# Performance work log

Hardware: AMD Instinct MI355X
Metric: run time of the kernel (lower is better)

The kernel has to match this reference:

```python
import jax, jax.numpy as jnp
import numpy as np
from jax import lax

IN_DIM = 256
MID = IN_DIM // 2          # 128
NUM_FILTERS = 8
OUT_DIM = 256
EMBED_DIM = 256
BN_EPS = 1e-5


def star_relu(x, scale, bias):
    # StarReLU: s * relu(x)**2 + b
    return scale * jnp.square(jax.nn.relu(x)) + bias


def setup_inputs() -> dict:
    key = jax.random.key(0)
    ks = jax.random.split(key, 12)
    B, H, W = 2, 16, 16
    h, w = 128, 128
    inp = {
        "x": jax.random.normal(ks[0], (B, IN_DIM, H, W), jnp.float32),
        "y": jax.random.normal(ks[1], (B, OUT_DIM, h, w), jnp.float32),
        # feature_fuse: 1x1 conv, depthwise 3x3 conv, BatchNorm (eval-mode stats)
        "conv1_w": jax.random.normal(ks[2], (MID, IN_DIM), jnp.float32) * 0.02,
        "conv1_b": jnp.zeros((MID,), jnp.float32),
        "dw_w": jax.random.normal(ks[3], (MID, 3, 3), jnp.float32) * 0.02,
        "dw_b": jnp.zeros((MID,), jnp.float32),
        "bn_gamma": jnp.ones((MID,), jnp.float32),
        "bn_beta": jnp.zeros((MID,), jnp.float32),
        "bn_mean": jax.random.normal(ks[4], (MID,), jnp.float32) * 0.1,
        "bn_var": jax.random.uniform(ks[5], (MID,), jnp.float32, 0.5, 1.5),
        "sr1_scale": jnp.ones((1,), jnp.float32),
        "sr1_bias": jnp.zeros((1,), jnp.float32),
        # channle_expand 1x1 conv
        "ce_w": jax.random.normal(ks[6], (NUM_FILTERS, MID), jnp.float32) * 0.02,
        "ce_b": jnp.zeros((NUM_FILTERS,), jnp.float32),
        "sr2_scale": jnp.ones((1,), jnp.float32),
        "sr2_bias": jnp.zeros((1,), jnp.float32),
        "W_base": jax.random.normal(ks[7], (OUT_DIM * EMBED_DIM, NUM_FILTERS), jnp.float32) * 0.02,
    }
    return inp


def reference(x, y, conv1_w, conv1_b, dw_w, dw_b, bn_gamma, bn_beta, bn_mean,
              bn_var, sr1_scale, sr1_bias, ce_w, ce_b, sr2_scale, sr2_bias, W_base):
    B, _, fh, fw = x.shape
    b, c, h, w = y.shape
    ph, pw = h // fh, w // fw

    # feature_fuse
    t = jnp.einsum('bchw,oc->bohw', x, conv1_w) + conv1_b[None, :, None, None]
    t = lax.conv_general_dilated(
        t, dw_w[:, None, :, :], (1, 1), ((1, 1), (1, 1)),
        feature_group_count=MID,
        dimension_numbers=('NCHW', 'OIHW', 'NCHW')) + dw_b[None, :, None, None]
    t = bn_gamma[None, :, None, None] * (t - bn_mean[None, :, None, None]) \
        * lax.rsqrt(bn_var + BN_EPS)[None, :, None, None] + bn_beta[None, :, None, None]
    t = star_relu(t, sr1_scale, sr1_bias)

    # channle_expand + act -> per-location filter coefficients [b, F, fh, fw]
    wdec = star_relu(jnp.einsum('bchw,fc->bfhw', t, ce_w) + ce_b[None, :, None, None],
                     sr2_scale, sr2_bias)

    # hypernetwork: [b, E*O, fh, fw], flattened as (embed_dim, out_dim)
    Wd = jnp.einsum('bfhw,ef->behw', wdec, W_base)
    Wd = Wd.reshape(b, EMBED_DIM, OUT_DIM, fh, fw)

    # massive-group 1x1 conv == per-(batch, block) small GEMM over spatial patches
    yb = y.reshape(b, c, fh, ph, fw, pw)
    out = jnp.einsum('beoij,boipjq->beipjq', Wd, yb)  # [b, E, fh, ph, fw, pw]
    return out.reshape(b, EMBED_DIM, h, w)
```

## Files before the change

### kernel.cpp

```cpp
#include <hip/hip_runtime.h>
#include <stdint.h>

typedef unsigned short u16t;
typedef unsigned int   u32t;
typedef __attribute__((ext_vector_type(8))) short short8;
typedef __attribute__((ext_vector_type(4))) float f32x4;

__device__ __forceinline__ float bf2f(u16t h){
  union { u32t u; float f; } c; c.u = ((u32t)h) << 16; return c.f;
}
__device__ __forceinline__ u16t f2bf(float f){
  union { float f; u32t u; } c; c.f = f;
  u32t u = c.u;
  u = u + 0x7fffu + ((u >> 16) & 1u);
  return (u16t)(u >> 16);
}
__device__ __forceinline__ u32t pk2(float a, float b){
  return (u32t)f2bf(a) | ((u32t)f2bf(b) << 16);
}

template<bool BF>
__device__ __forceinline__ float ldv(const void* p, size_t i){
  if constexpr (BF) return bf2f(((const u16t*)p)[i]);
  else              return ((const float*)p)[i];
}
template<bool BF>
__device__ __forceinline__ void ld8(const void* p, size_t i, float* v){
  if constexpr (BF){
    uint4 u = *(const uint4*)((const u16t*)p + i);
    const u32t a[4] = {u.x, u.y, u.z, u.w};
#pragma unroll
    for (int d = 0; d < 4; ++d){
      v[2*d]   = bf2f((u16t)(a[d] & 0xffffu));
      v[2*d+1] = bf2f((u16t)(a[d] >> 16));
    }
  } else {
    const float4* q = (const float4*)((const float*)p + i);
    float4 A = q[0], B = q[1];
    v[0]=A.x; v[1]=A.y; v[2]=A.z; v[3]=A.w;
    v[4]=B.x; v[5]=B.y; v[6]=B.z; v[7]=B.w;
  }
}
template<bool BF>
__device__ __forceinline__ void ld8pk(const void* p, size_t i, u32t* dst){
  if constexpr (BF){
    uint4 u = *(const uint4*)((const u16t*)p + i);
    dst[0]=u.x; dst[1]=u.y; dst[2]=u.z; dst[3]=u.w;
  } else {
    const float4* q = (const float4*)((const float*)p + i);
    float4 A = q[0], B = q[1];
    dst[0] = pk2(A.x, A.y); dst[1] = pk2(A.z, A.w);
    dst[2] = pk2(B.x, B.y); dst[3] = pk2(B.z, B.w);
  }
}

__global__ void k_probe(const void* xv, int* flag){
  __shared__ int cnt;
  const int t = threadIdx.x;
  if (t == 0) cnt = 0;
  __syncthreads();
  u16t h = ((const u16t*)xv)[t];
  int e = (h >> 7) & 0xff;
  if (e >= 90 && e <= 150) atomicAdd(&cnt, 1);
  __syncthreads();
  if (t == 0) *flag = (cnt >= 104) ? 1 : 0;
}

template<bool BF>
__device__ __forceinline__ void conv1_body(
    const void* x, const void* w, const void* bias, float* t1)
{
  __shared__ float xs[256];
  const int bid = blockIdx.x;
  const int b = bid >> 8, i = (bid >> 4) & 15, j = bid & 15;
  const int t = threadIdx.x;
  const size_t base = (size_t)b * 65536 + i * 16 + j;
  xs[t]       = ldv<BF>(x, base + (size_t)t * 256);
  xs[t + 128] = ldv<BF>(x, base + (size_t)(t + 128) * 256);
  __syncthreads();
  float acc = ldv<BF>(bias, t);
  for (int k = 0; k < 256; k += 8){
    float wv[8];
    ld8<BF>(w, (size_t)t * 256 + k, wv);
#pragma unroll
    for (int d = 0; d < 8; ++d) acc += xs[k + d] * wv[d];
  }
  t1[((size_t)(b * 128 + t) * 16 + i) * 16 + j] = acc;
}
__global__ __launch_bounds__(128) void k_conv1(
    const void* x, const void* w, const void* bias, float* t1, const int* flag){
  if (*flag) conv1_body<true >(x, w, bias, t1);
  else       conv1_body<false>(x, w, bias, t1);
}

template<bool BF>
__device__ __forceinline__ void wdec_body(
    const float* t1, const void* dww, const void* dwb,
    const void* bng, const void* bnb, const void* bnm, const void* bnv,
    const void* s1s, const void* s1b, const void* cew, const void* ceb,
    const void* s2s, const void* s2b, float* wdec)
{
  __shared__ float vs[128];
  const int bid = blockIdx.x;
  const int b = bid >> 8, i = (bid >> 4) & 15, j = bid & 15;
  const int c = threadIdx.x;
  float s = ldv<BF>(dwb, c);
  const float* tb = t1 + (size_t)(b * 128 + c) * 256;
#pragma unroll
  for (int di = 0; di < 3; ++di){
    const int ii = i + di - 1;
    if (ii < 0 || ii > 15) continue;
#pragma unroll
    for (int dj = 0; dj < 3; ++dj){
      const int jj = j + dj - 1;
      if (jj < 0 || jj > 15) continue;
      s += tb[ii * 16 + jj] * ldv<BF>(dww, c * 9 + di * 3 + dj);
    }
  }
  float v = ldv<BF>(bng, c) * (s - ldv<BF>(bnm, c)) *
            rsqrtf(ldv<BF>(bnv, c) + 1e-5f) + ldv<BF>(bnb, c);
  float rl = fmaxf(v, 0.0f);
  vs[c] = ldv<BF>(s1s, 0) * rl * rl + ldv<BF>(s1b, 0);
  __syncthreads();
  if (c < 8){
    float a = ldv<BF>(ceb, c);
    for (int k = 0; k < 128; ++k) a += vs[k] * ldv<BF>(cew, c * 128 + k);
    float r2 = fmaxf(a, 0.0f);
    wdec[bid * 8 + c] = ldv<BF>(s2s, 0) * r2 * r2 + ldv<BF>(s2b, 0);
  }
}
__global__ __launch_bounds__(128) void k_wdec(
    const float* t1, const void* dww, const void* dwb,
    const void* bng, const void* bnb, const void* bnm, const void* bnv,
    const void* s1s, const void* s1b, const void* cew, const void* ceb,
    const void* s2s, const void* s2b, float* wdec, const int* flag){
  if (*flag) wdec_body<true >(t1,dww,dwb,bng,bnb,bnm,bnv,s1s,s1b,cew,ceb,s2s,s2b,wdec);
  else       wdec_body<false>(t1,dww,dwb,bng,bnb,bnm,bnv,s1s,s1b,cew,ceb,s2s,s2b,wdec);
}

template<bool BF>
__device__ __forceinline__ void main_body(
    const void* y, const void* wbase, const float* wdec, void* out, u16t* smem)
{
  const int gx  = blockIdx.x;
  const int ec  = blockIdx.y;
  const int b   = gx >> 6;
  const int i   = (gx >> 2) & 15;
  const int j0  = (gx & 3) * 4;
  const int tid = threadIdx.x;

  {
    const int o_oct = tid & 31;
    const int p     = tid >> 5;
#pragma unroll
    for (int g = 0; g < 4; ++g){
      u32t Rp[8][4];
#pragma unroll
      for (int r = 0; r < 8; ++r){
        const size_t idx = (((size_t)(b * 256 + o_oct * 8 + r)) * 128 + (i * 8 + p)) * 128
                         + (j0 + g) * 8;
        ld8pk<BF>(y, idx, Rp[r]);
      }
#pragma unroll
      for (int q = 0; q < 8; ++q){
        const int d = q >> 1, h = q & 1;
        u32t cc[4];
#pragma unroll
        for (int k = 0; k < 4; ++k){
          const u32t lo32 = Rp[2*k][d], hi32 = Rp[2*k+1][d];
          cc[k] = h ? ((lo32 >> 16)     | (hi32 & 0xffff0000u))
                    : ((lo32 & 0xffffu) | (hi32 << 16));
        }
        const int row  = g * 64 + p * 8 + q;
        const int phys = (o_oct * 8 + row * 8) & 255;
        *(uint4*)(smem + row * 256 + phys) = make_uint4(cc[0], cc[1], cc[2], cc[3]);
      }
    }
  }
  __syncthreads();

  float wd[4][8];
#pragma unroll
  for (int g = 0; g < 4; ++g){
    const float* wp = wdec + (size_t)(b * 256 + i * 16 + j0 + g) * 8;
#pragma unroll
    for (int f = 0; f < 8; ++f) wd[g][f] = wp[f];
  }

  const int wave = tid >> 6, lane = tid & 63;
  const int l15 = lane & 15, l4 = lane >> 4;
  const int e_a = ec * 64 + wave * 16 + l15;
  const size_t wb_off = (size_t)e_a * 2048 + (size_t)l4 * 64;

  f32x4 acc[4][4];
#pragma unroll
  for (int g = 0; g < 4; ++g)
#pragma unroll
    for (int nt = 0; nt < 4; ++nt)
      acc[g][nt] = (f32x4){0.f, 0.f, 0.f, 0.f};

  u32t Wb[2][8][4];
#pragma unroll
  for (int m = 0; m < 8; ++m) ld8pk<BF>(wbase, wb_off + m * 8, Wb[0][m]);

#pragma unroll
  for (int ks = 0; ks < 8; ++ks){
    const int cur = ks & 1;
    if (ks < 7){
#pragma unroll
      for (int m = 0; m < 8; ++m)
        ld8pk<BF>(wbase, wb_off + (size_t)(ks + 1) * 256 + m * 8, Wb[cur ^ 1][m]);
    }
    float s[4][8];
#pragma unroll
    for (int m = 0; m < 8; ++m){
      float wf[8];
#pragma unroll
      for (int d = 0; d < 4; ++d){
        wf[2*d]   = bf2f((u16t)(Wb[cur][m][d] & 0xffffu));
        wf[2*d+1] = bf2f((u16t)(Wb[cur][m][d] >> 16));
      }
#pragma unroll
      for (int g = 0; g < 4; ++g){
        float t = 0.f;
#pragma unroll
        for (int f = 0; f < 8; ++f) t += wf[f] * wd[g][f];
        s[g][m] = t;
      }
    }
#pragma unroll
    for (int g = 0; g < 4; ++g){
      short8 af;
#pragma unroll
      for (int m = 0; m < 8; ++m) af[m] = (short)f2bf(s[g][m]);
#pragma unroll
      for (int nt = 0; nt < 4; ++nt){
        const int row = g * 64 + nt * 16 + l15;
        const int c0  = (ks * 32 + l4 * 8 + row * 8) & 255;
        const short8 bfr = *(const short8*)(smem + row * 256 + c0);
        acc[g][nt] = __builtin_amdgcn_mfma_f32_16x16x32_bf16(af, bfr, acc[g][nt], 0, 0, 0);
      }
    }
  }

#pragma unroll
  for (int g = 0; g < 4; ++g){
#pragma unroll
    for (int nt = 0; nt < 4; ++nt){
      const int col = nt * 16 + l15;
      const int pp = col >> 3, qq = col & 7;
#pragma unroll
      for (int r = 0; r < 4; ++r){
        const int ee = ec * 64 + wave * 16 + l4 * 4 + r;
        const size_t oaddr = ((size_t)(b * 256 + ee) * 128 + (i * 8 + pp)) * 128
                           + (j0 + g) * 8 + qq;
        const float v = acc[g][nt][r];
        if constexpr (BF) ((u16t*)out)[oaddr] = f2bf(v);
        else              ((float*)out)[oaddr] = v;
      }
    }
  }
}
__global__ __launch_bounds__(256, 1) void k_main(
    const void* y, const void* wbase, const float* wdec, void* out, const int* flag){
  extern __shared__ __align__(16) u16t smem[];
  if (*flag) main_body<true >(y, wbase, wdec, out, smem);
  else       main_body<false>(y, wbase, wdec, out, smem);
}

extern "C" void kernel_launch(void* const* d_in, const int* in_sizes, int n_in,
                              void* d_out, int out_size, void* d_ws, size_t ws_size,
                              hipStream_t stream)
{
  float* t1   = (float*)d_ws;
  float* wdec = (float*)d_ws + 65536;
  int*   flag = (int*)((char*)d_ws + 278528);

  k_probe<<<dim3(1), dim3(128), 0, stream>>>(d_in[0], flag);
  k_conv1<<<dim3(512), dim3(128), 0, stream>>>(d_in[0], d_in[2], d_in[3], t1, flag);
  k_wdec<<<dim3(512), dim3(128), 0, stream>>>(t1, d_in[4], d_in[5], d_in[6], d_in[7],
                                              d_in[8], d_in[9], d_in[10], d_in[11],
                                              d_in[12], d_in[13], d_in[14], d_in[15],
                                              wdec, flag);

  const int lds_bytes = 4 * 64 * 256 * 2;
  hipFuncSetAttribute((const void*)k_main,
                      hipFuncAttributeMaxDynamicSharedMemorySize, lds_bytes);
  k_main<<<dim3(128, 4), dim3(256), lds_bytes, stream>>>(d_in[1], d_in[16], wdec,
                                                         d_out, flag);
}
```

Measured before the change: 191.3 us.

## Fuse preprocessing kernels, pre-convert W_base to fp16 dot2, widen main blocks

Merges the 1x1 conv, depthwise conv, BN and StarReLU into one kernel, and computes the channel-expand in a separate small kernel that also writes fp16-packed filter coefficients. When the workspace is large enough, it adds a kernel that converts W_base to packed fp16 so the main kernel can use fdot2 instead of unpacking bf16 to float for the hypernetwork weights. The main kernel now uses 512-thread blocks covering 128 embed channels, halving the grid and reusing the staged y tile across twice as many outputs. The trade-offs are an fp16 precision change for the weights, an extra conversion pass over W_base on every call, and fewer but larger blocks.

```diff
diff --git a/kernel.cpp b/kernel.cpp
--- a/kernel.cpp
+++ b/kernel.cpp
@@ -3,8 +3,26 @@
 
 typedef unsigned short u16t;
 typedef unsigned int   u32t;
+typedef _Float16       h16;
+typedef __attribute__((ext_vector_type(2))) _Float16 h16x2;
 typedef __attribute__((ext_vector_type(8))) short short8;
 typedef __attribute__((ext_vector_type(4))) float f32x4;
+
+#if defined(__has_builtin)
+#if __has_builtin(__builtin_amdgcn_fdot2)
+#define HAVE_DOT2 1
+#endif
+#endif
+
+__device__ __forceinline__ float dot2h(u32t a, u32t b, float c){
+#ifdef HAVE_DOT2
+  return __builtin_amdgcn_fdot2(__builtin_bit_cast(h16x2, a),
+                                __builtin_bit_cast(h16x2, b), c, false);
+#else
+  h16x2 ha = __builtin_bit_cast(h16x2, a), hb = __builtin_bit_cast(h16x2, b);
+  return c + (float)ha[0]*(float)hb[0] + (float)ha[1]*(float)hb[1];
+#endif
+}
 
 __device__ __forceinline__ float bf2f(u16t h){
   union { u32t u; float f; } c; c.u = ((u32t)h) << 16; return c.f;
@@ -15,8 +33,12 @@
   u = u + 0x7fffu + ((u >> 16) & 1u);
   return (u16t)(u >> 16);
 }
-__device__ __forceinline__ u32t pk2(float a, float b){
+__device__ __forceinline__ u32t pk2bf(float a, float b){
   return (u32t)f2bf(a) | ((u32t)f2bf(b) << 16);
+}
+__device__ __forceinline__ u32t pk2h(float a, float b){
+  h16x2 h = { (h16)a, (h16)b };
+  return __builtin_bit_cast(u32t, h);
 }
 
 template<bool BF>
@@ -49,8 +71,8 @@
   } else {
     const float4* q = (const float4*)((const float*)p + i);
     float4 A = q[0], B = q[1];
-    dst[0] = pk2(A.x, A.y); dst[1] = pk2(A.z, A.w);
-    dst[2] = pk2(B.x, B.y); dst[3] = pk2(B.z, B.w);
+    dst[0] = pk2bf(A.x, A.y); dst[1] = pk2bf(A.z, A.w);
+    dst[2] = pk2bf(B.x, B.y); dst[3] = pk2bf(B.z, B.w);
   }
 }
 
@@ -67,80 +89,112 @@
 }
 
 template<bool BF>
-__device__ __forceinline__ void conv1_body(
-    const void* x, const void* w, const void* bias, float* t1)
+__device__ __forceinline__ void pre12_body(
+    const void* x, const void* w, const void* bias,
+    const void* dww, const void* dwb,
+    const void* bng, const void* bnb, const void* bnm, const void* bnv,
+    const void* s1s, const void* s1b, float* t2)
 {
-  __shared__ float xs[256];
-  const int bid = blockIdx.x;
-  const int b = bid >> 8, i = (bid >> 4) & 15, j = bid & 15;
-  const int t = threadIdx.x;
-  const size_t base = (size_t)b * 65536 + i * 16 + j;
-  xs[t]       = ldv<BF>(x, base + (size_t)t * 256);
-  xs[t + 128] = ldv<BF>(x, base + (size_t)(t + 128) * 256);
+  __shared__ float ts[2][256];
+  const int cg = blockIdx.x, b = blockIdx.y;
+  const int ij = threadIdx.x, i = ij >> 4, j = ij & 15;
+  const int c0 = cg * 2;
+  float a0 = ldv<BF>(bias, c0), a1 = ldv<BF>(bias, c0 + 1);
+  const size_t xb = (size_t)b * 65536 + ij;
+#pragma unroll 8
+  for (int k = 0; k < 256; ++k){
+    const float xv = ldv<BF>(x, xb + (size_t)k * 256);
+    a0 += xv * ldv<BF>(w, (size_t)c0 * 256 + k);
+    a1 += xv * ldv<BF>(w, (size_t)(c0 + 1) * 256 + k);
+  }
+  ts[0][ij] = a0;
+  ts[1][ij] = a1;
   __syncthreads();
-  float acc = ldv<BF>(bias, t);
-  for (int k = 0; k < 256; k += 8){
-    float wv[8];
-    ld8<BF>(w, (size_t)t * 256 + k, wv);
-#pragma unroll
-    for (int d = 0; d < 8; ++d) acc += xs[k + d] * wv[d];
-  }
-  t1[((size_t)(b * 128 + t) * 16 + i) * 16 + j] = acc;
-}
-__global__ __launch_bounds__(128) void k_conv1(
-    const void* x, const void* w, const void* bias, float* t1, const int* flag){
-  if (*flag) conv1_body<true >(x, w, bias, t1);
-  else       conv1_body<false>(x, w, bias, t1);
-}
-
-template<bool BF>
-__device__ __forceinline__ void wdec_body(
-    const float* t1, const void* dww, const void* dwb,
+  const float sc1 = ldv<BF>(s1s, 0), sb1 = ldv<BF>(s1b, 0);
+#pragma unroll
+  for (int cc = 0; cc < 2; ++cc){
+    const int c = c0 + cc;
+    float s = ldv<BF>(dwb, c);
+#pragma unroll
+    for (int di = 0; di < 3; ++di){
+      const int ii = i + di - 1;
+      if (ii < 0 || ii > 15) continue;
+#pragma unroll
+      for (int dj = 0; dj < 3; ++dj){
+        const int jj = j + dj - 1;
+        if (jj < 0 || jj > 15) continue;
+        s += ts[cc][ii * 16 + jj] * ldv<BF>(dww, c * 9 + di * 3 + dj);
+      }
+    }
+    const float v = ldv<BF>(bng, c) * (s - ldv<BF>(bnm, c)) *
+                    rsqrtf(ldv<BF>(bnv, c) + 1e-5f) + ldv<BF>(bnb, c);
+    const float r = fmaxf(v, 0.0f);
+    t2[((size_t)b * 128 + c) * 256 + ij] = sc1 * r * r + sb1;
+  }
+}
+__global__ __launch_bounds__(256) void k_pre12(
+    const void* x, const void* w, const void* bias,
+    const void* dww, const void* dwb,
     const void* bng, const void* bnb, const void* bnm, const void* bnv,
-    const void* s1s, const void* s1b, const void* cew, const void* ceb,
-    const void* s2s, const void* s2b, float* wdec)
+    const void* s1s, const void* s1b, float* t2, const int* flag){
+  if (*flag) pre12_body<true >(x,w,bias,dww,dwb,bng,bnb,bnm,bnv,s1s,s1b,t2);
+  else       pre12_body<false>(x,w,bias,dww,dwb,bng,bnb,bnm,bnv,s1s,s1b,t2);
+}
+
+template<bool BF>
+__device__ __forceinline__ void pre3_body(
+    const float* t2, const void* cew, const void* ceb,
+    const void* s2s, const void* s2b, float* wdecf, uint4* wdech)
 {
-  __shared__ float vs[128];
-  const int bid = blockIdx.x;
-  const int b = bid >> 8, i = (bid >> 4) & 15, j = bid & 15;
-  const int c = threadIdx.x;
-  float s = ldv<BF>(dwb, c);
-  const float* tb = t1 + (size_t)(b * 128 + c) * 256;
-#pragma unroll
-  for (int di = 0; di < 3; ++di){
-    const int ii = i + di - 1;
-    if (ii < 0 || ii > 15) continue;
-#pragma unroll
-    for (int dj = 0; dj < 3; ++dj){
-      const int jj = j + dj - 1;
-      if (jj < 0 || jj > 15) continue;
-      s += tb[ii * 16 + jj] * ldv<BF>(dww, c * 9 + di * 3 + dj);
-    }
-  }
-  float v = ldv<BF>(bng, c) * (s - ldv<BF>(bnm, c)) *
-            rsqrtf(ldv<BF>(bnv, c) + 1e-5f) + ldv<BF>(bnb, c);
-  float rl = fmaxf(v, 0.0f);
-  vs[c] = ldv<BF>(s1s, 0) * rl * rl + ldv<BF>(s1b, 0);
-  __syncthreads();
-  if (c < 8){
-    float a = ldv<BF>(ceb, c);
-    for (int k = 0; k < 128; ++k) a += vs[k] * ldv<BF>(cew, c * 128 + k);
-    float r2 = fmaxf(a, 0.0f);
-    wdec[bid * 8 + c] = ldv<BF>(s2s, 0) * r2 * r2 + ldv<BF>(s2b, 0);
-  }
-}
-__global__ __launch_bounds__(128) void k_wdec(
-    const float* t1, const void* dww, const void* dwb,
-    const void* bng, const void* bnb, const void* bnm, const void* bnv,
-    const void* s1s, const void* s1b, const void* cew, const void* ceb,
-    const void* s2s, const void* s2b, float* wdec, const int* flag){
-  if (*flag) wdec_body<true >(t1,dww,dwb,bng,bnb,bnm,bnv,s1s,s1b,cew,ceb,s2s,s2b,wdec);
-  else       wdec_body<false>(t1,dww,dwb,bng,bnb,bnm,bnv,s1s,s1b,cew,ceb,s2s,s2b,wdec);
-}
-
-template<bool BF>
+  const int b = blockIdx.x, ij = threadIdx.x;
+  float a[8];
+#pragma unroll
+  for (int f = 0; f < 8; ++f) a[f] = ldv<BF>(ceb, f);
+#pragma unroll 4
+  for (int c = 0; c < 128; ++c){
+    const float tv = t2[((size_t)b * 128 + c) * 256 + ij];
+#pragma unroll
+    for (int f = 0; f < 8; ++f) a[f] += tv * ldv<BF>(cew, f * 128 + c);
+  }
+  const float sc2 = ldv<BF>(s2s, 0), sb2 = ldv<BF>(s2b, 0);
+  float o[8];
+#pragma unroll
+  for (int f = 0; f < 8; ++f){
+    const float r = fmaxf(a[f], 0.0f);
+    o[f] = sc2 * r * r + sb2;
+  }
+  const int idx = b * 256 + ij;
+#pragma unroll
+  for (int f = 0; f < 8; ++f) wdecf[idx * 8 + f] = o[f];
+  if (wdech){
+    wdech[idx] = make_uint4(pk2h(o[0], o[1]), pk2h(o[2], o[3]),
+                            pk2h(o[4], o[5]), pk2h(o[6], o[7]));
+  }
+}
+__global__ __launch_bounds__(256) void k_pre3(
+    const float* t2, const void* cew, const void* ceb,
+    const void* s2s, const void* s2b, float* wdecf, uint4* wdech, const int* flag){
+  if (*flag) pre3_body<true >(t2, cew, ceb, s2s, s2b, wdecf, wdech);
+  else       pre3_body<false>(t2, cew, ceb, s2s, s2b, wdecf, wdech);
+}
+
+template<bool BF>
+__device__ __forceinline__ void prew_body(const void* wb, uint4* wbh){
+  const int t = blockIdx.x * 256 + threadIdx.x;
+  float v[8];
+  ld8<BF>(wb, (size_t)t * 8, v);
+  wbh[t] = make_uint4(pk2h(v[0], v[1]), pk2h(v[2], v[3]),
+                      pk2h(v[4], v[5]), pk2h(v[6], v[7]));
+}
+__global__ __launch_bounds__(256) void k_prew(const void* wb, uint4* wbh, const int* flag){
+  if (*flag) prew_body<true >(wb, wbh);
+  else       prew_body<false>(wb, wbh);
+}
+
+template<bool BF, bool PREW>
 __device__ __forceinline__ void main_body(
-    const void* y, const void* wbase, const float* wdec, void* out, u16t* smem)
+    const void* y, const void* wbase, const uint4* wbh,
+    const float* wdecf, const uint4* wdech, void* out, u16t* smem)
 {
   const int gx  = blockIdx.x;
   const int ec  = blockIdx.y;
@@ -151,9 +205,11 @@
 
   {
     const int o_oct = tid & 31;
-    const int p     = tid >> 5;
-#pragma unroll
-    for (int g = 0; g < 4; ++g){
+    const int p     = (tid >> 5) & 7;
+    const int gh    = tid >> 8;
+#pragma unroll
+    for (int gi = 0; gi < 2; ++gi){
+      const int g = gh * 2 + gi;
       u32t Rp[8][4];
 #pragma unroll
       for (int r = 0; r < 8; ++r){
@@ -179,18 +235,24 @@
   }
   __syncthreads();
 
-  float wd[4][8];
-#pragma unroll
-  for (int g = 0; g < 4; ++g){
-    const float* wp = wdec + (size_t)(b * 256 + i * 16 + j0 + g) * 8;
-#pragma unroll
-    for (int f = 0; f < 8; ++f) wd[g][f] = wp[f];
-  }
-
   const int wave = tid >> 6, lane = tid & 63;
   const int l15 = lane & 15, l4 = lane >> 4;
-  const int e_a = ec * 64 + wave * 16 + l15;
-  const size_t wb_off = (size_t)e_a * 2048 + (size_t)l4 * 64;
+  const int e0  = ec * 128 + wave * 16;
+  const int e_a = e0 + l15;
+
+  u32t wdp[4][4];
+  float wdf[4][8];
+#pragma unroll
+  for (int g = 0; g < 4; ++g){
+    const int loc = b * 256 + i * 16 + j0 + g;
+    if constexpr (PREW){
+      const uint4 q = wdech[loc];
+      wdp[g][0] = q.x; wdp[g][1] = q.y; wdp[g][2] = q.z; wdp[g][3] = q.w;
+    } else {
+#pragma unroll
+      for (int f = 0; f < 8; ++f) wdf[g][f] = wdecf[loc * 8 + f];
+    }
+  }
 
   f32x4 acc[4][4];
 #pragma unroll
@@ -199,33 +261,59 @@
     for (int nt = 0; nt < 4; ++nt)
       acc[g][nt] = (f32x4){0.f, 0.f, 0.f, 0.f};
 
+  const uint4* wb4 = wbh + (size_t)e_a * 256 + l4 * 8;
+  const size_t wb_off = (size_t)e_a * 2048 + (size_t)l4 * 64;
+
   u32t Wb[2][8][4];
 #pragma unroll
-  for (int m = 0; m < 8; ++m) ld8pk<BF>(wbase, wb_off + m * 8, Wb[0][m]);
+  for (int m = 0; m < 8; ++m){
+    if constexpr (PREW){
+      const uint4 q = wb4[m];
+      Wb[0][m][0]=q.x; Wb[0][m][1]=q.y; Wb[0][m][2]=q.z; Wb[0][m][3]=q.w;
+    } else {
+      ld8pk<BF>(wbase, wb_off + m * 8, Wb[0][m]);
+    }
+  }
 
 #pragma unroll
   for (int ks = 0; ks < 8; ++ks){
     const int cur = ks & 1;
     if (ks < 7){
 #pragma unroll
-      for (int m = 0; m < 8; ++m)
-        ld8pk<BF>(wbase, wb_off + (size_t)(ks + 1) * 256 + m * 8, Wb[cur ^ 1][m]);
+      for (int m = 0; m < 8; ++m){
+        if constexpr (PREW){
+          const uint4 q = wb4[(ks + 1) * 32 + m];
+          Wb[cur^1][m][0]=q.x; Wb[cur^1][m][1]=q.y; Wb[cur^1][m][2]=q.z; Wb[cur^1][m][3]=q.w;
+        } else {
+          ld8pk<BF>(wbase, wb_off + (size_t)(ks + 1) * 256 + m * 8, Wb[cur^1][m]);
+        }
+      }
     }
     float s[4][8];
 #pragma unroll
     for (int m = 0; m < 8; ++m){
-      float wf[8];
-#pragma unroll
-      for (int d = 0; d < 4; ++d){
-        wf[2*d]   = bf2f((u16t)(Wb[cur][m][d] & 0xffffu));
-        wf[2*d+1] = bf2f((u16t)(Wb[cur][m][d] >> 16));
-      }
-#pragma unroll
-      for (int g = 0; g < 4; ++g){
-        float t = 0.f;
-#pragma unroll
-        for (int f = 0; f < 8; ++f) t += wf[f] * wd[g][f];
-        s[g][m] = t;
+      if constexpr (PREW){
+#pragma unroll
+        for (int g = 0; g < 4; ++g){
+          float t = 0.f;
+#pragma unroll
+          for (int d = 0; d < 4; ++d) t = dot2h(Wb[cur][m][d], wdp[g][d], t);
+          s[g][m] = t;
+        }
+      } else {
+        float wf[8];
+#pragma unroll
+        for (int d = 0; d < 4; ++d){
+          wf[2*d]   = bf2f((u16t)(Wb[cur][m][d] & 0xffffu));
+          wf[2*d+1] = bf2f((u16t)(Wb[cur][m][d] >> 16));
+        }
+#pragma unroll
+        for (int g = 0; g < 4; ++g){
+          float t = 0.f;
+#pragma unroll
+          for (int f = 0; f < 8; ++f) t += wf[f] * wdf[g][f];
+          s[g][m] = t;
+        }
       }
     }
 #pragma unroll
@@ -251,7 +339,7 @@
       const int pp = col >> 3, qq = col & 7;
 #pragma unroll
       for (int r = 0; r < 4; ++r){
-        const int ee = ec * 64 + wave * 16 + l4 * 4 + r;
+        const int ee = e0 + l4 * 4 + r;
         const size_t oaddr = ((size_t)(b * 256 + ee) * 128 + (i * 8 + pp)) * 128
                            + (j0 + g) * 8 + qq;
         const float v = acc[g][nt][r];
@@ -261,31 +349,50 @@
     }
   }
 }
-__global__ __launch_bounds__(256, 1) void k_main(
-    const void* y, const void* wbase, const float* wdec, void* out, const int* flag){
+
+__global__ __launch_bounds__(512, 2) void k_main_pw(
+    const void* y, const uint4* wbh, const uint4* wdech, void* out, const int* flag){
   extern __shared__ __align__(16) u16t smem[];
-  if (*flag) main_body<true >(y, wbase, wdec, out, smem);
-  else       main_body<false>(y, wbase, wdec, out, smem);
+  if (*flag) main_body<true , true>(y, nullptr, wbh, nullptr, wdech, out, smem);
+  else       main_body<false, true>(y, nullptr, wbh, nullptr, wdech, out, smem);
+}
+__global__ __launch_bounds__(512, 2) void k_main_npw(
+    const void* y, const void* wbase, const float* wdecf, void* out, const int* flag){
+  extern __shared__ __align__(16) u16t smem[];
+  if (*flag) main_body<true , false>(y, wbase, nullptr, wdecf, nullptr, out, smem);
+  else       main_body<false, false>(y, wbase, nullptr, wdecf, nullptr, out, smem);
 }
 
 extern "C" void kernel_launch(void* const* d_in, const int* in_sizes, int n_in,
                               void* d_out, int out_size, void* d_ws, size_t ws_size,
                               hipStream_t stream)
 {
-  float* t1   = (float*)d_ws;
-  float* wdec = (float*)d_ws + 65536;
-  int*   flag = (int*)((char*)d_ws + 278528);
+  float* t2    = (float*)d_ws;
+  float* wdecf = (float*)((char*)d_ws + 262144);
+  int*   flag  = (int*)((char*)d_ws + 278528);
+  uint4* wdech = (uint4*)((char*)d_ws + 278544);
+  uint4* wbh   = (uint4*)((char*)d_ws + 286736);
+  const bool prew = (ws_size >= 286736u + 1048576u);
 
   k_probe<<<dim3(1), dim3(128), 0, stream>>>(d_in[0], flag);
-  k_conv1<<<dim3(512), dim3(128), 0, stream>>>(d_in[0], d_in[2], d_in[3], t1, flag);
-  k_wdec<<<dim3(512), dim3(128), 0, stream>>>(t1, d_in[4], d_in[5], d_in[6], d_in[7],
-                                              d_in[8], d_in[9], d_in[10], d_in[11],
-                                              d_in[12], d_in[13], d_in[14], d_in[15],
-                                              wdec, flag);
+  k_pre12<<<dim3(64, 2), dim3(256), 0, stream>>>(
+      d_in[0], d_in[2], d_in[3], d_in[4], d_in[5], d_in[6], d_in[7],
+      d_in[8], d_in[9], d_in[10], d_in[11], t2, flag);
+  k_pre3<<<dim3(2), dim3(256), 0, stream>>>(
+      t2, d_in[12], d_in[13], d_in[14], d_in[15], wdecf,
+      prew ? wdech : (uint4*)nullptr, flag);
 
   const int lds_bytes = 4 * 64 * 256 * 2;
-  hipFuncSetAttribute((const void*)k_main,
-                      hipFuncAttributeMaxDynamicSharedMemorySize, lds_bytes);
-  k_main<<<dim3(128, 4), dim3(256), lds_bytes, stream>>>(d_in[1], d_in[16], wdec,
-                                                         d_out, flag);
-}
+  if (prew){
+    k_prew<<<dim3(256), dim3(256), 0, stream>>>(d_in[16], wbh, flag);
+    hipFuncSetAttribute((const void*)k_main_pw,
+                        hipFuncAttributeMaxDynamicSharedMemorySize, lds_bytes);
+    k_main_pw<<<dim3(128, 2), dim3(512), lds_bytes, stream>>>(
+        d_in[1], wbh, wdech, d_out, flag);
+  } else {
+    hipFuncSetAttribute((const void*)k_main_npw,
+                        hipFuncAttributeMaxDynamicSharedMemorySize, lds_bytes);
+    k_main_npw<<<dim3(128, 2), dim3(512), lds_bytes, stream>>>(
+        d_in[1], d_in[16], wdecf, d_out, flag);
+  }
+}
```

Result: faster. 179.5 us (-6.2%).
